# Kernel tuning notes

Hardware: AMD Instinct MI355X
Metric: run time of the kernel (lower is better)

The kernel has to match this reference:

```python
import jax, jax.numpy as jnp
import numpy as np

N_NODES, N_EDGES = 50000, 200000
DN, DE, DG = 256, 256, 128

def setup_inputs() -> dict:
    key = jax.random.key(0)
    ks = jax.random.split(key, 8)
    s = lambda d: 1.0 / np.sqrt(d)
    return {
        "nodes": jax.random.normal(ks[0], (N_NODES, DN), jnp.float32),
        "edges": jax.random.normal(ks[1], (N_EDGES, DE), jnp.float32),
        "globals_": jax.random.normal(ks[2], (DG,), jnp.float32),
        "senders": jax.random.randint(ks[3], (N_EDGES,), 0, N_NODES, jnp.int32),
        "receivers": jax.random.randint(ks[4], (N_EDGES,), 0, N_NODES, jnp.int32),
        "We": jax.random.normal(ks[5], (DE + 2 * DN + DG, DE), jnp.float32) * s(DE + 2 * DN + DG),
        "be": jnp.zeros((DE,), jnp.float32),
        "Wn": jax.random.normal(ks[6], (DE + DN + DG, DN), jnp.float32) * s(DE + DN + DG),
        "bn": jnp.zeros((DN,), jnp.float32),
        "Wg": jax.random.normal(ks[7], (DE + DN + DG, DG), jnp.float32) * s(DE + DN + DG),
        "bg": jnp.zeros((DG,), jnp.float32),
    }

def reference(nodes, edges, globals_, senders, receivers, We, be, Wn, bn, Wg, bg):
    E, N = edges.shape[0], nodes.shape[0]
    # --- edge processor: phi_e([e, v_s, v_r, u]) ---
    edge_in = jnp.concatenate(
        [edges, nodes[senders], nodes[receivers],
         jnp.broadcast_to(globals_, (E, globals_.shape[0]))], axis=-1)  # [E, 896]
    new_edges = jax.nn.relu(edge_in @ We + be)  # [E, DE]
    # --- node processor: phi_v([sum_incoming_e, v, u]) ---
    agg_e = jax.ops.segment_sum(new_edges, receivers, num_segments=N)  # [N, DE]
    node_in = jnp.concatenate(
        [agg_e, nodes, jnp.broadcast_to(globals_, (N, globals_.shape[0]))], axis=-1)
    new_nodes = jax.nn.relu(node_in @ Wn + bn)  # [N, DN]
    # --- global processor: phi_u([sum_e, sum_v, u]) ---
    global_in = jnp.concatenate(
        [new_edges.sum(axis=0), new_nodes.sum(axis=0), globals_], axis=-1)
    new_globals = jax.nn.relu(global_in @ Wg + bg)  # [DG]
    return new_edges, new_nodes, new_globals
```

## Files before the change

### kernel.cpp

```cpp
#include <hip/hip_runtime.h>

#define E_CNT 200000
#define N_CNT 50000
#define CS_PARTS 128

typedef __attribute__((ext_vector_type(8))) unsigned short ushort8;
typedef __attribute__((ext_vector_type(4))) unsigned short us4;
typedef __attribute__((ext_vector_type(4))) float f32x4;
typedef __bf16 bf16x8 __attribute__((ext_vector_type(8)));

static __device__ __forceinline__ unsigned short f2bf(float f) {
  unsigned int u = __builtin_bit_cast(unsigned int, f);
  u += 0x7FFFu + ((u >> 16) & 1u);
  return (unsigned short)(u >> 16);
}
static __device__ __forceinline__ float bf2f(unsigned short u) {
  unsigned int x = ((unsigned int)u) << 16;
  return __builtin_bit_cast(float, x);
}

__global__ void prep_all(const float* __restrict__ We, const float* __restrict__ be,
                         const float* __restrict__ Wn, const float* __restrict__ bn,
                         const float* __restrict__ g, unsigned short* __restrict__ BpEe,
                         unsigned short* __restrict__ BpPs, unsigned short* __restrict__ BpPr,
                         unsigned short* __restrict__ BpN, float* __restrict__ ce,
                         float* __restrict__ cn) {
  int bid = blockIdx.x;
  if (bid >= 160) {
    int j = threadIdx.x;
    if (bid == 160) {
      float s = be[j];
      for (int k = 0; k < 128; ++k) s += g[k] * We[(size_t)(768 + k) * 256 + j];
      ce[j] = s;
    } else {
      float s = bn[j];
      for (int k = 0; k < 128; ++k) s += g[k] * Wn[(size_t)(512 + k) * 256 + j];
      cn[j] = s;
    }
    return;
  }
  int sub = bid >> 5;
  const float* W;
  unsigned short* Bp;
  if (sub == 0)      { W = We;           Bp = BpEe; }
  else if (sub == 1) { W = We + 65536;   Bp = BpPs; }
  else if (sub == 2) { W = We + 131072;  Bp = BpPr; }
  else if (sub == 3) { W = Wn;           Bp = BpN; }
  else               { W = Wn + 65536;   Bp = BpN + 65536; }
  int idx = (bid & 31) * 256 + threadIdx.x;
  int lane = idx & 63;
  int t = idx >> 6;
  int F = t & 15;
  int kc = t >> 4;
  int col = F * 16 + (lane & 15);
  int kb = kc * 32 + (lane >> 4) * 8;
  ushort8 v;
#pragma unroll
  for (int j = 0; j < 8; ++j) v[j] = f2bf(W[(size_t)(kb + j) * 256 + col]);
  *reinterpret_cast<ushort8*>(Bp + (size_t)idx * 8) = v;
}

__global__ __launch_bounds__(512, 4) void proj2(
    const float* __restrict__ nodes, const unsigned short* __restrict__ BpPs,
    const unsigned short* __restrict__ BpPr, unsigned short* __restrict__ Ps,
    unsigned short* __restrict__ Pr) {
  __shared__ unsigned short ldsA[4][64 * 64];

  const int tid = threadIdx.x;
  const int lane = tid & 63;
  const int wave = tid >> 6;
  const int wm = wave >> 2;
  const int wn = wave & 3;
  const int q = lane >> 4;
  const int lr = lane & 15;
  const int row0 = blockIdx.x * 64;

  const int sr = tid >> 3;
  const int sc = tid & 7;
  int er = row0 + sr;
  if (er > N_CNT - 1) er = N_CNT - 1;
  const float* sbase = nodes + (size_t)er * 256;
  const int swz = sr & 7;
  const int wbase = sr * 64;
  const int s0 = (sc ^ swz) * 8;

#pragma unroll
  for (int ks = 0; ks < 4; ++ks) {
    f32x4 f0 = *reinterpret_cast<const f32x4*>(sbase + ks * 64 + sc * 8);
    f32x4 f1 = *reinterpret_cast<const f32x4*>(sbase + ks * 64 + sc * 8 + 4);
    ushort8 w0;
#pragma unroll
    for (int j = 0; j < 4; ++j) {
      w0[j] = f2bf(f0[j]);
      w0[4 + j] = f2bf(f1[j]);
    }
    *reinterpret_cast<ushort8*>(&ldsA[ks][wbase + s0]) = w0;
  }
  __syncthreads();

  auto do_proj = [&](const unsigned short* __restrict__ Bp,
                     unsigned short* __restrict__ outP) {
    f32x4 acc[2][4] = {};
#pragma unroll
    for (int ks = 0; ks < 4; ++ks) {
#pragma unroll
      for (int kk = 0; kk < 2; ++kk) {
        const int kc32 = ks * 2 + kk;
        bf16x8 bfr[4];
#pragma unroll
        for (int fn = 0; fn < 4; ++fn) {
          const int F = wn * 4 + fn;
          bfr[fn] = __builtin_bit_cast(
              bf16x8, *reinterpret_cast<const ushort8*>(
                          Bp + ((size_t)(kc32 * 16 + F) * 64 + lane) * 8));
        }
        bf16x8 a[2];
#pragma unroll
        for (int fm = 0; fm < 2; ++fm) {
          int r = wm * 32 + fm * 16 + lr;
          int slot = (kk * 4 + q) ^ (r & 7);
          a[fm] = __builtin_bit_cast(
              bf16x8, *reinterpret_cast<const ushort8*>(&ldsA[ks][r * 64 + slot * 8]));
        }
#pragma unroll
        for (int fm = 0; fm < 2; ++fm)
#pragma unroll
          for (int fn = 0; fn < 4; ++fn)
            acc[fm][fn] = __builtin_amdgcn_mfma_f32_16x16x32_bf16(
                a[fm], bfr[fn], acc[fm][fn], 0, 0, 0);
      }
    }
#pragma unroll
    for (int fm = 0; fm < 2; ++fm) {
      int rb = row0 + wm * 32 + fm * 16 + q * 4;
#pragma unroll
      for (int i = 0; i < 4; ++i) {
        int gr = rb + i;
        if (gr < N_CNT) {
          us4 pv;
#pragma unroll
          for (int fn = 0; fn < 4; ++fn) pv[fn] = f2bf(acc[fm][fn][i]);
          *reinterpret_cast<us4*>(outP + (size_t)gr * 256 + wn * 64 + lr * 4) = pv;
        }
      }
    }
  };

  do_proj(BpPs, Ps);
  do_proj(BpPr, Pr);
}

__global__ __launch_bounds__(512, 2) void edge_gemm(
    const float* __restrict__ edges, const unsigned short* __restrict__ BpEe,
    const unsigned short* __restrict__ Ps, const unsigned short* __restrict__ Pr,
    const float* __restrict__ ce, const int* __restrict__ senders,
    const int* __restrict__ receivers, float* __restrict__ out0,
    float* __restrict__ agg, float* __restrict__ partE) {
  __shared__ unsigned short lds[2][128 * 64];

  const int tid = threadIdx.x;
  const int lane = tid & 63;
  const int wave = tid >> 6;
  const int wm = wave >> 2;
  const int wn = wave & 3;
  const int q = lane >> 4;
  const int lr = lane & 15;
  const int row0 = blockIdx.x * 128;

  const int sr = tid >> 2;
  const int sc = tid & 3;
  int er = row0 + sr;
  if (er > E_CNT - 1) er = E_CNT - 1;
  const float* sbase = edges + (size_t)er * 256;

  const int swz = sr & 7;
  const int wbase = sr * 64;
  const int s0 = ((sc * 2) ^ swz) * 8;
  const int s1 = ((sc * 2 + 1) ^ swz) * 8;

  f32x4 acc[4][4] = {};

  {
    const float4* p4 = reinterpret_cast<const float4*>(sbase + sc * 16);
    float fv[16];
    *reinterpret_cast<float4*>(&fv[0]) = p4[0];
    *reinterpret_cast<float4*>(&fv[4]) = p4[1];
    *reinterpret_cast<float4*>(&fv[8]) = p4[2];
    *reinterpret_cast<float4*>(&fv[12]) = p4[3];
    ushort8 w0, w1;
#pragma unroll
    for (int j = 0; j < 8; ++j) {
      w0[j] = f2bf(fv[j]);
      w1[j] = f2bf(fv[8 + j]);
    }
    *reinterpret_cast<ushort8*>(&lds[0][wbase + s0]) = w0;
    *reinterpret_cast<ushort8*>(&lds[0][wbase + s1]) = w1;
  }
  __syncthreads();

#pragma unroll
  for (int ks = 0; ks < 4; ++ks) {
    const int cc = ks & 1;

    bf16x8 bfr[2][4];
#pragma unroll
    for (int kk = 0; kk < 2; ++kk) {
      const int kc32 = ks * 2 + kk;
#pragma unroll
      for (int fn = 0; fn < 4; ++fn) {
        const int F = wn * 4 + fn;
        bfr[kk][fn] = __builtin_bit_cast(
            bf16x8, *reinterpret_cast<const ushort8*>(
                        BpEe + ((size_t)(kc32 * 16 + F) * 64 + lane) * 8));
      }
    }

    float4 nf0, nf1, nf2, nf3;
    if (ks + 1 < 4) {
      const float4* p4 = reinterpret_cast<const float4*>(sbase + (ks + 1) * 64 + sc * 16);
      nf0 = p4[0];
      nf1 = p4[1];
      nf2 = p4[2];
      nf3 = p4[3];
    }

#pragma unroll
    for (int kk = 0; kk < 2; ++kk) {
      bf16x8 a[4];
#pragma unroll
      for (int fm = 0; fm < 4; ++fm) {
        int r = wm * 64 + fm * 16 + lr;
        int slot = (kk * 4 + q) ^ (r & 7);
        a[fm] = __builtin_bit_cast(
            bf16x8, *reinterpret_cast<const ushort8*>(&lds[cc][r * 64 + slot * 8]));
      }
#pragma unroll
      for (int fm = 0; fm < 4; ++fm)
#pragma unroll
        for (int fn = 0; fn < 4; ++fn)
          acc[fm][fn] = __builtin_amdgcn_mfma_f32_16x16x32_bf16(
              a[fm], bfr[kk][fn], acc[fm][fn], 0, 0, 0);
    }

    if (ks + 1 < 4) {
      float fv[16];
      *reinterpret_cast<float4*>(&fv[0]) = nf0;
      *reinterpret_cast<float4*>(&fv[4]) = nf1;
      *reinterpret_cast<float4*>(&fv[8]) = nf2;
      *reinterpret_cast<float4*>(&fv[12]) = nf3;
      ushort8 w0, w1;
#pragma unroll
      for (int j = 0; j < 8; ++j) {
        w0[j] = f2bf(fv[j]);
        w1[j] = f2bf(fv[8 + j]);
      }
      *reinterpret_cast<ushort8*>(&lds[cc ^ 1][wbase + s0]) = w0;
      *reinterpret_cast<ushort8*>(&lds[cc ^ 1][wbase + s1]) = w1;
      __syncthreads();
    }
  }

  float bcol[4];
#pragma unroll
  for (int fn = 0; fn < 4; ++fn) bcol[fn] = ce[wn * 64 + fn * 16 + lr];
  float cs[4] = {0.f, 0.f, 0.f, 0.f};

#pragma unroll
  for (int fm = 0; fm < 4; ++fm) {
    int rb = row0 + wm * 64 + fm * 16 + q * 4;
#pragma unroll
    for (int i = 0; i < 4; ++i) {
      int gr = rb + i;
      if (gr < E_CNT) {
        int snd = senders[gr], rcv = receivers[gr];
        us4 ps = *reinterpret_cast<const us4*>(Ps + (size_t)snd * 256 + wn * 64 + lr * 4);
        us4 pr = *reinterpret_cast<const us4*>(Pr + (size_t)rcv * 256 + wn * 64 + lr * 4);
#pragma unroll
        for (int fn = 0; fn < 4; ++fn) {
          int col = wn * 64 + fn * 16 + lr;
          float v = fmaxf(acc[fm][fn][i] + bcol[fn] + bf2f(ps[fn]) + bf2f(pr[fn]), 0.0f);
          cs[fn] += v;
          __builtin_nontemporal_store(v, &out0[(size_t)gr * 256 + col]);
          atomicAdd(agg + (size_t)rcv * 256 + col, v);
        }
      }
    }
  }

  float* csum = reinterpret_cast<float*>(&lds[0][0]);
  __syncthreads();
  if (tid < 256) csum[tid] = 0.f;
  __syncthreads();
#pragma unroll
  for (int fn = 0; fn < 4; ++fn) atomicAdd(&csum[wn * 64 + fn * 16 + lr], cs[fn]);
  __syncthreads();
  if (tid < 256)
    atomicAdd(&partE[(size_t)(blockIdx.x & (CS_PARTS - 1)) * 256 + tid], csum[tid]);
}

__global__ __launch_bounds__(512, 2) void node_gemm(
    const float* __restrict__ agg, const float* __restrict__ nodes,
    const unsigned short* __restrict__ BpN, const float* __restrict__ cn,
    const float* __restrict__ partE, float* __restrict__ esum,
    float* __restrict__ out1, float* __restrict__ partN, int nbN) {
  if (blockIdx.x >= nbN) {
    int c = threadIdx.x;
    if (c < 256) {
      float s = 0.f;
      for (int p = 0; p < CS_PARTS; ++p) s += partE[(size_t)p * 256 + c];
      esum[c] = s;
    }
    return;
  }
  __shared__ unsigned short lds[2][128 * 64];

  const int tid = threadIdx.x;
  const int lane = tid & 63;
  const int wave = tid >> 6;
  const int wm = wave >> 2;
  const int wn = wave & 3;
  const int q = lane >> 4;
  const int lr = lane & 15;
  const int row0 = blockIdx.x * 128;

  const int sr = tid >> 2;
  const int sc = tid & 3;
  int er = row0 + sr;
  if (er > N_CNT - 1) er = N_CNT - 1;
  const float* sbase[2];
  sbase[0] = agg + (size_t)er * 256;
  sbase[1] = nodes + (size_t)er * 256;

  const int swz = sr & 7;
  const int wbase = sr * 64;
  const int s0 = ((sc * 2) ^ swz) * 8;
  const int s1 = ((sc * 2 + 1) ^ swz) * 8;

  f32x4 acc[4][4] = {};

  {
    const float4* p4 = reinterpret_cast<const float4*>(sbase[0] + sc * 16);
    float fv[16];
    *reinterpret_cast<float4*>(&fv[0]) = p4[0];
    *reinterpret_cast<float4*>(&fv[4]) = p4[1];
    *reinterpret_cast<float4*>(&fv[8]) = p4[2];
    *reinterpret_cast<float4*>(&fv[12]) = p4[3];
    ushort8 w0, w1;
#pragma unroll
    for (int j = 0; j < 8; ++j) {
      w0[j] = f2bf(fv[j]);
      w1[j] = f2bf(fv[8 + j]);
    }
    *reinterpret_cast<ushort8*>(&lds[0][wbase + s0]) = w0;
    *reinterpret_cast<ushort8*>(&lds[0][wbase + s1]) = w1;
  }
  __syncthreads();

#pragma unroll
  for (int ks = 0; ks < 8; ++ks) {
    const int cc = ks & 1;

    bf16x8 bfr[2][4];
#pragma unroll
    for (int kk = 0; kk < 2; ++kk) {
      const int kc32 = ks * 2 + kk;
#pragma unroll
      for (int fn = 0; fn < 4; ++fn) {
        const int F = wn * 4 + fn;
        bfr[kk][fn] = __builtin_bit_cast(
            bf16x8, *reinterpret_cast<const ushort8*>(
                        BpN + ((size_t)(kc32 * 16 + F) * 64 + lane) * 8));
      }
    }

    float4 nf0, nf1, nf2, nf3;
    if (ks + 1 < 8) {
      const float4* p4 = reinterpret_cast<const float4*>(
          sbase[(ks + 1) >> 2] + ((ks + 1) & 3) * 64 + sc * 16);
      nf0 = p4[0];
      nf1 = p4[1];
      nf2 = p4[2];
      nf3 = p4[3];
    }

#pragma unroll
    for (int kk = 0; kk < 2; ++kk) {
      bf16x8 a[4];
#pragma unroll
      for (int fm = 0; fm < 4; ++fm) {
        int r = wm * 64 + fm * 16 + lr;
        int slot = (kk * 4 + q) ^ (r & 7);
        a[fm] = __builtin_bit_cast(
            bf16x8, *reinterpret_cast<const ushort8*>(&lds[cc][r * 64 + slot * 8]));
      }
#pragma unroll
      for (int fm = 0; fm < 4; ++fm)
#pragma unroll
        for (int fn = 0; fn < 4; ++fn)
          acc[fm][fn] = __builtin_amdgcn_mfma_f32_16x16x32_bf16(
              a[fm], bfr[kk][fn], acc[fm][fn], 0, 0, 0);
    }

    if (ks + 1 < 8) {
      float fv[16];
      *reinterpret_cast<float4*>(&fv[0]) = nf0;
      *reinterpret_cast<float4*>(&fv[4]) = nf1;
      *reinterpret_cast<float4*>(&fv[8]) = nf2;
      *reinterpret_cast<float4*>(&fv[12]) = nf3;
      ushort8 w0, w1;
#pragma unroll
      for (int j = 0; j < 8; ++j) {
        w0[j] = f2bf(fv[j]);
        w1[j] = f2bf(fv[8 + j]);
      }
      *reinterpret_cast<ushort8*>(&lds[cc ^ 1][wbase + s0]) = w0;
      *reinterpret_cast<ushort8*>(&lds[cc ^ 1][wbase + s1]) = w1;
      __syncthreads();
    }
  }

  float bcol[4];
#pragma unroll
  for (int fn = 0; fn < 4; ++fn) bcol[fn] = cn[wn * 64 + fn * 16 + lr];
  float cs[4] = {0.f, 0.f, 0.f, 0.f};

#pragma unroll
  for (int fm = 0; fm < 4; ++fm) {
    int rb = row0 + wm * 64 + fm * 16 + q * 4;
#pragma unroll
    for (int i = 0; i < 4; ++i) {
      int gr = rb + i;
      if (gr < N_CNT) {
#pragma unroll
        for (int fn = 0; fn < 4; ++fn) {
          int col = wn * 64 + fn * 16 + lr;
          float v = fmaxf(acc[fm][fn][i] + bcol[fn], 0.0f);
          cs[fn] += v;
          out1[(size_t)gr * 256 + col] = v;
        }
      }
    }
  }

  float* csum = reinterpret_cast<float*>(&lds[0][0]);
  __syncthreads();
  if (tid < 256) csum[tid] = 0.f;
  __syncthreads();
#pragma unroll
  for (int fn = 0; fn < 4; ++fn) atomicAdd(&csum[wn * 64 + fn * 16 + lr], cs[fn]);
  __syncthreads();
  if (tid < 256)
    atomicAdd(&partN[(size_t)(blockIdx.x & (CS_PARTS - 1)) * 256 + tid], csum[tid]);
}

__global__ void finalize(const float* __restrict__ partN, const float* __restrict__ esum,
                         const float* __restrict__ gl, const float* __restrict__ Wg,
                         const float* __restrict__ bg, float* __restrict__ out2) {
  __shared__ float ns[256];
  __shared__ float red[512];
  int t = threadIdx.x;
  if (t < 256) {
    float s = 0.f;
    for (int p = 0; p < CS_PARTS; ++p) s += partN[(size_t)p * 256 + t];
    ns[t] = s;
  }
  __syncthreads();
  int g = t & 127;
  int kg = t >> 7;
  float acc = 0.f;
  for (int k = kg; k < 640; k += 4) {
    float x = (k < 256) ? esum[k] : (k < 512 ? ns[k - 256] : gl[k - 512]);
    acc += x * Wg[(size_t)k * 128 + g];
  }
  red[t] = acc;
  __syncthreads();
  if (kg == 0) {
    float r = red[g] + red[128 + g] + red[256 + g] + red[384 + g] + bg[g];
    out2[g] = fmaxf(r, 0.f);
  }
}

extern "C" void kernel_launch(void* const* d_in, const int* in_sizes, int n_in,
                              void* d_out, int out_size, void* d_ws, size_t ws_size,
                              hipStream_t stream) {
  const float* nodes = (const float*)d_in[0];
  const float* edges = (const float*)d_in[1];
  const float* gl = (const float*)d_in[2];
  const int* senders = (const int*)d_in[3];
  const int* receivers = (const int*)d_in[4];
  const float* We = (const float*)d_in[5];
  const float* be = (const float*)d_in[6];
  const float* Wn = (const float*)d_in[7];
  const float* bn = (const float*)d_in[8];
  const float* Wg = (const float*)d_in[9];
  const float* bg = (const float*)d_in[10];

  float* out0 = (float*)d_out;
  float* out1 = out0 + (size_t)E_CNT * 256;
  float* out2 = out1 + (size_t)N_CNT * 256;

  float* agg = out1;

  char* ws = (char*)d_ws;
  size_t o = 0;
  float* partE = (float*)(ws + o);                  o += CS_PARTS * 256 * 4;
  float* partN = (float*)(ws + o);                  o += CS_PARTS * 256 * 4;
  size_t zeroBytes = o;
  unsigned short* Ps = (unsigned short*)(ws + o);   o += (size_t)N_CNT * 256 * 2;
  unsigned short* Pr = (unsigned short*)(ws + o);   o += (size_t)N_CNT * 256 * 2;
  unsigned short* BpEe = (unsigned short*)(ws + o); o += 131072;
  unsigned short* BpPs = (unsigned short*)(ws + o); o += 131072;
  unsigned short* BpPr = (unsigned short*)(ws + o); o += 131072;
  unsigned short* BpN = (unsigned short*)(ws + o);  o += 262144;
  float* ce = (float*)(ws + o);                     o += 1024;
  float* cn = (float*)(ws + o);                     o += 1024;
  float* esum = (float*)(ws + o);                   o += 1024;

  hipMemsetAsync(ws, 0, zeroBytes, stream);
  hipMemsetAsync(agg, 0, (size_t)N_CNT * 256 * 4, stream);

  prep_all<<<162, 256, 0, stream>>>(We, be, Wn, bn, gl, BpEe, BpPs, BpPr, BpN, ce, cn);

  proj2<<<(N_CNT + 63) / 64, 512, 0, stream>>>(nodes, BpPs, BpPr, Ps, Pr);

  edge_gemm<<<(E_CNT + 127) / 128, 512, 0, stream>>>(
      edges, BpEe, Ps, Pr, ce, senders, receivers, out0, agg, partE);

  const int nbN = (N_CNT + 127) / 128;
  node_gemm<<<nbN + 1, 512, 0, stream>>>(agg, nodes, BpN, cn, partE, esum, out1,
                                         partN, nbN);

  finalize<<<1, 512, 0, stream>>>(partN, esum, gl, Wg, bg, out2);
}
```

Before: 473.7 us.

## Fold node self-projection into proj kernel and compute column sums separately

```diff
diff --git a/kernel.cpp b/kernel.cpp
--- a/kernel.cpp
+++ b/kernel.cpp
@@ -23,8 +23,8 @@
                          const float* __restrict__ Wn, const float* __restrict__ bn,
                          const float* __restrict__ g, unsigned short* __restrict__ BpEe,
                          unsigned short* __restrict__ BpPs, unsigned short* __restrict__ BpPr,
-                         unsigned short* __restrict__ BpN, float* __restrict__ ce,
-                         float* __restrict__ cn) {
+                         unsigned short* __restrict__ BpNe, unsigned short* __restrict__ BpPn,
+                         float* __restrict__ ce, float* __restrict__ cn) {
   int bid = blockIdx.x;
   if (bid >= 160) {
     int j = threadIdx.x;
@@ -45,8 +45,8 @@
   if (sub == 0)      { W = We;           Bp = BpEe; }
   else if (sub == 1) { W = We + 65536;   Bp = BpPs; }
   else if (sub == 2) { W = We + 131072;  Bp = BpPr; }
-  else if (sub == 3) { W = Wn;           Bp = BpN; }
-  else               { W = Wn + 65536;   Bp = BpN + 65536; }
+  else if (sub == 3) { W = Wn;           Bp = BpNe; }
+  else               { W = Wn + 65536;   Bp = BpPn; }
   int idx = (bid & 31) * 256 + threadIdx.x;
   int lane = idx & 63;
   int t = idx >> 6;
@@ -60,10 +60,11 @@
   *reinterpret_cast<ushort8*>(Bp + (size_t)idx * 8) = v;
 }
 
-__global__ __launch_bounds__(512, 4) void proj2(
+__global__ __launch_bounds__(512, 4) void proj3(
     const float* __restrict__ nodes, const unsigned short* __restrict__ BpPs,
-    const unsigned short* __restrict__ BpPr, unsigned short* __restrict__ Ps,
-    unsigned short* __restrict__ Pr) {
+    const unsigned short* __restrict__ BpPr, const unsigned short* __restrict__ BpPn,
+    unsigned short* __restrict__ Ps, unsigned short* __restrict__ Pr,
+    unsigned short* __restrict__ Pn) {
   __shared__ unsigned short ldsA[4][64 * 64];
 
   const int tid = threadIdx.x;
@@ -148,6 +149,7 @@
 
   do_proj(BpPs, Ps);
   do_proj(BpPr, Pr);
+  do_proj(BpPn, Pn);
 }
 
 __global__ __launch_bounds__(512, 2) void edge_gemm(
@@ -155,7 +157,7 @@
     const unsigned short* __restrict__ Ps, const unsigned short* __restrict__ Pr,
     const float* __restrict__ ce, const int* __restrict__ senders,
     const int* __restrict__ receivers, float* __restrict__ out0,
-    float* __restrict__ agg, float* __restrict__ partE) {
+    float* __restrict__ agg) {
   __shared__ unsigned short lds[2][128 * 64];
 
   const int tid = threadIdx.x;
@@ -263,8 +265,6 @@
   float bcol[4];
 #pragma unroll
   for (int fn = 0; fn < 4; ++fn) bcol[fn] = ce[wn * 64 + fn * 16 + lr];
-  float cs[4] = {0.f, 0.f, 0.f, 0.f};
-
 #pragma unroll
   for (int fm = 0; fm < 4; ++fm) {
     int rb = row0 + wm * 64 + fm * 16 + q * 4;
@@ -279,40 +279,19 @@
         for (int fn = 0; fn < 4; ++fn) {
           int col = wn * 64 + fn * 16 + lr;
           float v = fmaxf(acc[fm][fn][i] + bcol[fn] + bf2f(ps[fn]) + bf2f(pr[fn]), 0.0f);
-          cs[fn] += v;
           __builtin_nontemporal_store(v, &out0[(size_t)gr * 256 + col]);
           atomicAdd(agg + (size_t)rcv * 256 + col, v);
         }
       }
     }
   }
-
-  float* csum = reinterpret_cast<float*>(&lds[0][0]);
-  __syncthreads();
-  if (tid < 256) csum[tid] = 0.f;
-  __syncthreads();
-#pragma unroll
-  for (int fn = 0; fn < 4; ++fn) atomicAdd(&csum[wn * 64 + fn * 16 + lr], cs[fn]);
-  __syncthreads();
-  if (tid < 256)
-    atomicAdd(&partE[(size_t)(blockIdx.x & (CS_PARTS - 1)) * 256 + tid], csum[tid]);
-}
-
-__global__ __launch_bounds__(512, 2) void node_gemm(
-    const float* __restrict__ agg, const float* __restrict__ nodes,
-    const unsigned short* __restrict__ BpN, const float* __restrict__ cn,
-    const float* __restrict__ partE, float* __restrict__ esum,
-    float* __restrict__ out1, float* __restrict__ partN, int nbN) {
-  if (blockIdx.x >= nbN) {
-    int c = threadIdx.x;
-    if (c < 256) {
-      float s = 0.f;
-      for (int p = 0; p < CS_PARTS; ++p) s += partE[(size_t)p * 256 + c];
-      esum[c] = s;
-    }
-    return;
-  }
-  __shared__ unsigned short lds[2][128 * 64];
+}
+
+__global__ __launch_bounds__(512, 8) void node_gemm(
+    const float* __restrict__ agg, const unsigned short* __restrict__ BpNe,
+    const unsigned short* __restrict__ Pn, const float* __restrict__ cn,
+    float* __restrict__ out1) {
+  __shared__ unsigned short lds[2][64 * 64];
 
   const int tid = threadIdx.x;
   const int lane = tid & 63;
@@ -321,100 +300,77 @@
   const int wn = wave & 3;
   const int q = lane >> 4;
   const int lr = lane & 15;
-  const int row0 = blockIdx.x * 128;
-
-  const int sr = tid >> 2;
-  const int sc = tid & 3;
+  const int row0 = blockIdx.x * 64;
+
+  const int sr = tid >> 3;
+  const int sc = tid & 7;
   int er = row0 + sr;
   if (er > N_CNT - 1) er = N_CNT - 1;
-  const float* sbase[2];
-  sbase[0] = agg + (size_t)er * 256;
-  sbase[1] = nodes + (size_t)er * 256;
-
+  const float* sbase = agg + (size_t)er * 256;
   const int swz = sr & 7;
   const int wbase = sr * 64;
-  const int s0 = ((sc * 2) ^ swz) * 8;
-  const int s1 = ((sc * 2 + 1) ^ swz) * 8;
-
-  f32x4 acc[4][4] = {};
+  const int s0 = (sc ^ swz) * 8;
+
+  f32x4 acc[2][4] = {};
 
   {
-    const float4* p4 = reinterpret_cast<const float4*>(sbase[0] + sc * 16);
-    float fv[16];
-    *reinterpret_cast<float4*>(&fv[0]) = p4[0];
-    *reinterpret_cast<float4*>(&fv[4]) = p4[1];
-    *reinterpret_cast<float4*>(&fv[8]) = p4[2];
-    *reinterpret_cast<float4*>(&fv[12]) = p4[3];
-    ushort8 w0, w1;
-#pragma unroll
-    for (int j = 0; j < 8; ++j) {
-      w0[j] = f2bf(fv[j]);
-      w1[j] = f2bf(fv[8 + j]);
+    f32x4 f0 = *reinterpret_cast<const f32x4*>(sbase + sc * 8);
+    f32x4 f1 = *reinterpret_cast<const f32x4*>(sbase + sc * 8 + 4);
+    ushort8 w0;
+#pragma unroll
+    for (int j = 0; j < 4; ++j) {
+      w0[j] = f2bf(f0[j]);
+      w0[4 + j] = f2bf(f1[j]);
     }
     *reinterpret_cast<ushort8*>(&lds[0][wbase + s0]) = w0;
-    *reinterpret_cast<ushort8*>(&lds[0][wbase + s1]) = w1;
   }
   __syncthreads();
 
 #pragma unroll
-  for (int ks = 0; ks < 8; ++ks) {
+  for (int ks = 0; ks < 4; ++ks) {
     const int cc = ks & 1;
 
-    bf16x8 bfr[2][4];
+    f32x4 nf0, nf1;
+    if (ks + 1 < 4) {
+      nf0 = *reinterpret_cast<const f32x4*>(sbase + (ks + 1) * 64 + sc * 8);
+      nf1 = *reinterpret_cast<const f32x4*>(sbase + (ks + 1) * 64 + sc * 8 + 4);
+    }
+
 #pragma unroll
     for (int kk = 0; kk < 2; ++kk) {
       const int kc32 = ks * 2 + kk;
+      bf16x8 bfr[4];
 #pragma unroll
       for (int fn = 0; fn < 4; ++fn) {
         const int F = wn * 4 + fn;
-        bfr[kk][fn] = __builtin_bit_cast(
+        bfr[fn] = __builtin_bit_cast(
             bf16x8, *reinterpret_cast<const ushort8*>(
-                        BpN + ((size_t)(kc32 * 16 + F) * 64 + lane) * 8));
-      }
-    }
-
-    float4 nf0, nf1, nf2, nf3;
-    if (ks + 1 < 8) {
-      const float4* p4 = reinterpret_cast<const float4*>(
-          sbase[(ks + 1) >> 2] + ((ks + 1) & 3) * 64 + sc * 16);
-      nf0 = p4[0];
-      nf1 = p4[1];
-      nf2 = p4[2];
-      nf3 = p4[3];
-    }
-
-#pragma unroll
-    for (int kk = 0; kk < 2; ++kk) {
-      bf16x8 a[4];
-#pragma unroll
-      for (int fm = 0; fm < 4; ++fm) {
-        int r = wm * 64 + fm * 16 + lr;
+                        BpNe + ((size_t)(kc32 * 16 + F) * 64 + lane) * 8));
+      }
+      bf16x8 a[2];
+#pragma unroll
+      for (int fm = 0; fm < 2; ++fm) {
+        int r = wm * 32 + fm * 16 + lr;
         int slot = (kk * 4 + q) ^ (r & 7);
         a[fm] = __builtin_bit_cast(
             bf16x8, *reinterpret_cast<const ushort8*>(&lds[cc][r * 64 + slot * 8]));
       }
 #pragma unroll
-      for (int fm = 0; fm < 4; ++fm)
+      for (int fm = 0; fm < 2; ++fm)
 #pragma unroll
         for (int fn = 0; fn < 4; ++fn)
           acc[fm][fn] = __builtin_amdgcn_mfma_f32_16x16x32_bf16(
-              a[fm], bfr[kk][fn], acc[fm][fn], 0, 0, 0);
-    }
-
-    if (ks + 1 < 8) {
-      float fv[16];
-      *reinterpret_cast<float4*>(&fv[0]) = nf0;
-      *reinterpret_cast<float4*>(&fv[4]) = nf1;
-      *reinterpret_cast<float4*>(&fv[8]) = nf2;
-      *reinterpret_cast<float4*>(&fv[12]) = nf3;
-      ushort8 w0, w1;
-#pragma unroll
-      for (int j = 0; j < 8; ++j) {
-        w0[j] = f2bf(fv[j]);
-        w1[j] = f2bf(fv[8 + j]);
+              a[fm], bfr[fn], acc[fm][fn], 0, 0, 0);
+    }
+
+    if (ks + 1 < 4) {
+      ushort8 w0;
+#pragma unroll
+      for (int j = 0; j < 4; ++j) {
+        w0[j] = f2bf(nf0[j]);
+        w0[4 + j] = f2bf(nf1[j]);
       }
       *reinterpret_cast<ushort8*>(&lds[cc ^ 1][wbase + s0]) = w0;
-      *reinterpret_cast<ushort8*>(&lds[cc ^ 1][wbase + s1]) = w1;
       __syncthreads();
     }
   }
@@ -422,54 +378,63 @@
   float bcol[4];
 #pragma unroll
   for (int fn = 0; fn < 4; ++fn) bcol[fn] = cn[wn * 64 + fn * 16 + lr];
-  float cs[4] = {0.f, 0.f, 0.f, 0.f};
-
-#pragma unroll
-  for (int fm = 0; fm < 4; ++fm) {
-    int rb = row0 + wm * 64 + fm * 16 + q * 4;
+#pragma unroll
+  for (int fm = 0; fm < 2; ++fm) {
+    int rb = row0 + wm * 32 + fm * 16 + q * 4;
 #pragma unroll
     for (int i = 0; i < 4; ++i) {
       int gr = rb + i;
       if (gr < N_CNT) {
+        us4 pn = *reinterpret_cast<const us4*>(Pn + (size_t)gr * 256 + wn * 64 + lr * 4);
 #pragma unroll
         for (int fn = 0; fn < 4; ++fn) {
           int col = wn * 64 + fn * 16 + lr;
-          float v = fmaxf(acc[fm][fn][i] + bcol[fn], 0.0f);
-          cs[fn] += v;
-          out1[(size_t)gr * 256 + col] = v;
+          out1[(size_t)gr * 256 + col] =
+              fmaxf(acc[fm][fn][i] + bcol[fn] + bf2f(pn[fn]), 0.0f);
         }
       }
     }
   }
-
-  float* csum = reinterpret_cast<float*>(&lds[0][0]);
+}
+
+__global__ void colsum_p1(const float* __restrict__ in, float* __restrict__ part, int rows) {
+  const int c4 = threadIdx.x & 63;
+  const int rg = threadIdx.x >> 6;
+  f32x4 s = {0.f, 0.f, 0.f, 0.f};
+  for (int r = blockIdx.x * 4 + rg; r < rows; r += CS_PARTS * 4)
+    s += *reinterpret_cast<const f32x4*>(in + (size_t)r * 256 + c4 * 4);
+  __shared__ f32x4 red[256];
+  red[threadIdx.x] = s;
   __syncthreads();
-  if (tid < 256) csum[tid] = 0.f;
-  __syncthreads();
-#pragma unroll
-  for (int fn = 0; fn < 4; ++fn) atomicAdd(&csum[wn * 64 + fn * 16 + lr], cs[fn]);
-  __syncthreads();
-  if (tid < 256)
-    atomicAdd(&partN[(size_t)(blockIdx.x & (CS_PARTS - 1)) * 256 + tid], csum[tid]);
-}
-
-__global__ void finalize(const float* __restrict__ partN, const float* __restrict__ esum,
+  if (rg == 0) {
+    f32x4 r = red[c4] + red[64 + c4] + red[128 + c4] + red[192 + c4];
+    *reinterpret_cast<f32x4*>(part + (size_t)blockIdx.x * 256 + c4 * 4) = r;
+  }
+}
+
+__global__ void finalize(const float* __restrict__ partE, const float* __restrict__ partN,
                          const float* __restrict__ gl, const float* __restrict__ Wg,
                          const float* __restrict__ bg, float* __restrict__ out2) {
+  __shared__ float es[256];
   __shared__ float ns[256];
   __shared__ float red[512];
   int t = threadIdx.x;
   if (t < 256) {
     float s = 0.f;
-    for (int p = 0; p < CS_PARTS; ++p) s += partN[(size_t)p * 256 + t];
-    ns[t] = s;
+    for (int p = 0; p < CS_PARTS; ++p) s += partE[(size_t)p * 256 + t];
+    es[t] = s;
+  } else {
+    int c = t - 256;
+    float s = 0.f;
+    for (int p = 0; p < CS_PARTS; ++p) s += partN[(size_t)p * 256 + c];
+    ns[c] = s;
   }
   __syncthreads();
   int g = t & 127;
   int kg = t >> 7;
   float acc = 0.f;
   for (int k = kg; k < 640; k += 4) {
-    float x = (k < 256) ? esum[k] : (k < 512 ? ns[k - 256] : gl[k - 512]);
+    float x = (k < 256) ? es[k] : (k < 512 ? ns[k - 256] : gl[k - 512]);
     acc += x * Wg[(size_t)k * 128 + g];
   }
   red[t] = acc;
@@ -508,27 +473,31 @@
   size_t zeroBytes = o;
   unsigned short* Ps = (unsigned short*)(ws + o);   o += (size_t)N_CNT * 256 * 2;
   unsigned short* Pr = (unsigned short*)(ws + o);   o += (size_t)N_CNT * 256 * 2;
+  unsigned short* Pn = (unsigned short*)(ws + o);   o += (size_t)N_CNT * 256 * 2;
   unsigned short* BpEe = (unsigned short*)(ws + o); o += 131072;
   unsigned short* BpPs = (unsigned short*)(ws + o); o += 131072;
   unsigned short* BpPr = (unsigned short*)(ws + o); o += 131072;
-  unsigned short* BpN = (unsigned short*)(ws + o);  o += 262144;
+  unsigned short* BpNe = (unsigned short*)(ws + o); o += 131072;
+  unsigned short* BpPn = (unsigned short*)(ws + o); o += 131072;
   float* ce = (float*)(ws + o);                     o += 1024;
   float* cn = (float*)(ws + o);                     o += 1024;
-  float* esum = (float*)(ws + o);                   o += 1024;
 
   hipMemsetAsync(ws, 0, zeroBytes, stream);
   hipMemsetAsync(agg, 0, (size_t)N_CNT * 256 * 4, stream);
 
-  prep_all<<<162, 256, 0, stream>>>(We, be, Wn, bn, gl, BpEe, BpPs, BpPr, BpN, ce, cn);
-
-  proj2<<<(N_CNT + 63) / 64, 512, 0, stream>>>(nodes, BpPs, BpPr, Ps, Pr);
+  prep_all<<<162, 256, 0, stream>>>(We, be, Wn, bn, gl, BpEe, BpPs, BpPr, BpNe,
+                                    BpPn, ce, cn);
+
+  proj3<<<(N_CNT + 63) / 64, 512, 0, stream>>>(nodes, BpPs, BpPr, BpPn, Ps, Pr, Pn);
 
   edge_gemm<<<(E_CNT + 127) / 128, 512, 0, stream>>>(
-      edges, BpEe, Ps, Pr, ce, senders, receivers, out0, agg, partE);
-
-  const int nbN = (N_CNT + 127) / 128;
-  node_gemm<<<nbN + 1, 512, 0, stream>>>(agg, nodes, BpN, cn, partE, esum, out1,
-                                         partN, nbN);
-
-  finalize<<<1, 512, 0, stream>>>(partN, esum, gl, Wg, bg, out2);
-}
+      edges, BpEe, Ps, Pr, ce, senders, receivers, out0, agg);
+
+  colsum_p1<<<CS_PARTS, 256, 0, stream>>>(agg, partE, N_CNT);
+
+  node_gemm<<<(N_CNT + 63) / 64, 512, 0, stream>>>(agg, BpNe, Pn, cn, out1);
+
+  colsum_p1<<<CS_PARTS, 256, 0, stream>>>(out1, partN, N_CNT);
+
+  finalize<<<1, 512, 0, stream>>>(partE, partN, gl, Wg, bg, out2);
+}
```

Result: slower. 548.3 us (+15.7%).
